# Kernel optimization log

Hardware: AMD Instinct MI355X
Metric: run time of the kernel (lower is better)

Reference implementation:

```python
import jax, jax.numpy as jnp
import numpy as np

HEAD_DIM = 128
NUM_Q_HEAD = 32
NUM_KV_HEAD = 8
SEQLEN_Q = 4096
SEQLEN_KV = 4096
BLOCK_Q = 128
BLOCK_KV = 128
WINDOW = 512
SOFTMAX_CAP = 50.0
EPS = 1e-5
SCALE = 1.0 / np.sqrt(HEAD_DIM)


def group_rms_norm(x, gamma, group_size, eps):
    # x: [b, s, hidden]; RMS-normalize each contiguous group of `group_size` channels, then scale by gamma
    b, s, h = x.shape
    xg = x.reshape(b, s, h // group_size, group_size)
    rms = jnp.sqrt(jnp.mean(jnp.square(xg), axis=-1, keepdims=True) + eps)
    return (xg / rms).reshape(b, s, h) * gamma


def setup_inputs() -> dict:
    key = jax.random.key(0)
    ks = jax.random.split(key, 7)
    b = 4
    q = jax.random.normal(ks[0], (b, BLOCK_Q, NUM_Q_HEAD, HEAD_DIM), dtype=jnp.float32)
    k = jax.random.normal(ks[1], (b, BLOCK_KV, NUM_KV_HEAD, HEAD_DIM), dtype=jnp.float32)
    v = jax.random.normal(ks[2], (b, BLOCK_KV, NUM_KV_HEAD, HEAD_DIM), dtype=jnp.float32)
    global_o = jax.random.normal(ks[3], (b, SEQLEN_Q, NUM_Q_HEAD, HEAD_DIM), dtype=jnp.float32)
    global_lse = jax.random.normal(ks[4], (b, NUM_Q_HEAD, SEQLEN_Q), dtype=jnp.float32)
    gq = jax.random.uniform(ks[5], (NUM_Q_HEAD * HEAD_DIM,), dtype=jnp.float32, minval=-1.0, maxval=1.0)
    gk = jax.random.uniform(ks[6], (NUM_KV_HEAD * HEAD_DIM,), dtype=jnp.float32, minval=-1.0, maxval=1.0)
    return {"q": q, "k": k, "v": v, "global_o": global_o, "global_lse": global_lse,
            "gq": gq, "gk": gk, "block_idx_q": 16, "block_idx_kv": 13}


def reference(q, k, v, global_o, global_lse, gq, gk, block_idx_q, block_idx_kv):
    b, bq = q.shape[0], q.shape[1]
    bkv = k.shape[1]
    # fused QK GroupRMSNorm (group_size == head_dim -> per-head RMS)
    qn = group_rms_norm(q.reshape(b, bq, -1), gq, HEAD_DIM, EPS).reshape(q.shape)
    kn = group_rms_norm(k.reshape(b, bkv, -1), gk, HEAD_DIM, EPS).reshape(k.shape)
    # GQA: repeat kv heads
    rep = NUM_Q_HEAD // NUM_KV_HEAD
    kr = jnp.repeat(kn, rep, axis=2)  # [b, bkv, Hq, d]
    vr = jnp.repeat(v, rep, axis=2)
    # block logits with softmax capping
    logits = jnp.einsum('bqhd,bkhd->bhqk', qn, kr) * SCALE
    logits = SOFTMAX_CAP * jnp.tanh(logits / SOFTMAX_CAP)
    # global positions + causal/sliding-window/padding mask
    qi = block_idx_q * bq + jnp.arange(bq)      # [bq]
    kj = block_idx_kv * bkv + jnp.arange(bkv)   # [bkv]
    offset = SEQLEN_KV - SEQLEN_Q
    diag = qi[:, None] + offset
    allowed = (kj[None, :] <= diag) & (kj[None, :] >= diag - WINDOW)
    allowed = allowed & (qi[:, None] < SEQLEN_Q) & (kj[None, :] < SEQLEN_KV)
    logits = jnp.where(allowed[None, None], logits, -jnp.inf)
    # local softmax stats
    lse_blk = jax.nn.logsumexp(logits, axis=-1)             # [b, h, bq]
    p = jnp.exp(logits - lse_blk[..., None])
    p = jnp.where(jnp.isfinite(lse_blk)[..., None], p, 0.0)  # fully-masked rows -> 0
    o_blk = jnp.einsum('bhqk,bkhd->bqhd', p, vr)             # [b, bq, h, d]
    # online merge with running stats
    row0 = block_idx_q * bq
    lse_old = jax.lax.dynamic_slice_in_dim(global_lse, row0, bq, axis=2)  # [b, h, bq]
    o_old = jax.lax.dynamic_slice_in_dim(global_o, row0, bq, axis=1)      # [b, bq, h, d]
    lse_new = jnp.logaddexp(lse_old, lse_blk)
    fin = jnp.isfinite(lse_new)
    c_old = jnp.where(fin, jnp.exp(jnp.where(fin, lse_old - lse_new, 0.0)), 0.0)
    c_blk = jnp.where(fin, jnp.exp(jnp.where(fin, lse_blk - lse_new, 0.0)), 0.0)
    o_new = jnp.transpose(c_old, (0, 2, 1))[..., None] * o_old + jnp.transpose(c_blk, (0, 2, 1))[..., None] * o_blk
    global_o = jax.lax.dynamic_update_slice_in_dim(global_o, o_new, row0, axis=1)
    global_lse = jax.lax.dynamic_update_slice_in_dim(global_lse, lse_new, row0, axis=2)
    return global_o, global_lse
```

## Files before the change

### kernel.cpp

```cpp
#include <hip/hip_runtime.h>
#include <math.h>

#define HEAD_DIM   128
#define NUM_Q_HEAD 32
#define NUM_KV_HEAD 8
#define SEQLEN_Q   4096
#define SEQLEN_KV  4096
#define BLOCK_Q    128
#define BLOCK_KV   128
#define WINDOW     512
#define SOFTCAP    50.0f
#define EPSV       1e-5f
#define NB         4

#define QROWS  32
#define ZSPLIT (BLOCK_Q / QROWS)
#define NATT   (NB * NUM_Q_HEAD * ZSPLIT)

#define O_FLOATS   (NB * SEQLEN_Q * NUM_Q_HEAD * HEAD_DIM)
#define LSE_FLOATS (NB * NUM_Q_HEAD * SEQLEN_Q)
#define O4N   (O_FLOATS / 4)
#define L4N   (LSE_FLOATS / 4)

#define GRID_COPY 2048
#define GSIZE     ((long long)GRID_COPY * 256)

__global__ __launch_bounds__(256) void bulk_copy(
    const float* __restrict__ gog, const float* __restrict__ glse,
    float* __restrict__ out)
{
    const float4* so = (const float4*)gog;
    const float4* sl = (const float4*)glse;
    float4* d0 = (float4*)out;
    float4* dL = (float4*)(out + (long long)O_FLOATS);

    const long long g = (long long)blockIdx.x * 256 + threadIdx.x;

#pragma unroll
    for (int it = 0; it < 8; ++it) {
        const long long i = g + (long long)it * (GSIZE * 4);
        float4 a = so[i];
        float4 b = so[i + GSIZE];
        float4 c = so[i + 2 * GSIZE];
        float4 d = so[i + 3 * GSIZE];
        d0[i]             = a;
        d0[i + GSIZE]     = b;
        d0[i + 2 * GSIZE] = c;
        d0[i + 3 * GSIZE] = d;
    }
    if (g < (long long)L4N) dL[g] = sl[g];
}

__global__ __launch_bounds__(256, 2) void osw_attn(
    const float* __restrict__ qg, const float* __restrict__ kg_,
    const float* __restrict__ vg, const float* __restrict__ gog,
    const float* __restrict__ glse, const float* __restrict__ gq,
    const float* __restrict__ gk, const int* __restrict__ pbq,
    const int* __restrict__ pbkv, float* __restrict__ out)
{
    __shared__ float kv[64][HEAD_DIM + 4];
    __shared__ float buf[QROWS][HEAD_DIM + 4];
    __shared__ float invks[BLOCK_KV];

    const int tid  = threadIdx.x;
    const int row0 = pbq[0] * BLOCK_Q;

    const int ab = blockIdx.x;
    const int b  = ab >> 7;
    const int h  = (ab >> 2) & 31;
    const int z  = ab & 3;
    const int qo = z * QROWS;
    const int kh = h >> 2;
    const int blkkv = pbkv[0];
    const float scale = 0.088388347648318447f;

    {
        const int r = tid >> 1, half = tid & 1;
        const float* kr = kg_ + (((long long)b * BLOCK_KV + r) * NUM_KV_HEAD + kh) * HEAD_DIM + half * 64;
        float ss = 0.f;
#pragma unroll
        for (int i = 0; i < 16; ++i) {
            float4 x = ((const float4*)kr)[i];
            ss = fmaf(x.x, x.x, ss); ss = fmaf(x.y, x.y, ss);
            ss = fmaf(x.z, x.z, ss); ss = fmaf(x.w, x.w, ss);
        }
        ss += __shfl_xor(ss, 1);
        if (half == 0) invks[r] = rsqrtf(ss * (1.0f / HEAD_DIM) + EPSV);
    }

    {
        const int r = tid >> 3, part = tid & 7;
        const float* qr = qg + (((long long)b * BLOCK_Q + qo + r) * NUM_Q_HEAD + h) * HEAD_DIM + part * 16;
        float4 xv[4];
        float ss = 0.f;
#pragma unroll
        for (int i = 0; i < 4; ++i) {
            xv[i] = ((const float4*)qr)[i];
            ss = fmaf(xv[i].x, xv[i].x, ss); ss = fmaf(xv[i].y, xv[i].y, ss);
            ss = fmaf(xv[i].z, xv[i].z, ss); ss = fmaf(xv[i].w, xv[i].w, ss);
        }
        ss += __shfl_xor(ss, 1);
        ss += __shfl_xor(ss, 2);
        ss += __shfl_xor(ss, 4);
        const float inv = rsqrtf(ss * (1.0f / HEAD_DIM) + EPSV) * scale;
        const float* gqp = gq + h * HEAD_DIM + part * 16;
        const float* gkp = gk + kh * HEAD_DIM + part * 16;
#pragma unroll
        for (int i = 0; i < 4; ++i) {
            float4 a = ((const float4*)gqp)[i];
            float4 c = ((const float4*)gkp)[i];
            int d = part * 16 + i * 4;
            buf[r][d + 0] = xv[i].x * inv * a.x * c.x;
            buf[r][d + 1] = xv[i].y * inv * a.y * c.y;
            buf[r][d + 2] = xv[i].z * inv * a.z * c.z;
            buf[r][d + 3] = xv[i].w * inv * a.w * c.w;
        }
    }
    __syncthreads();

    const int qrow = tid >> 3;
    const int l8   = tid & 7;
    const int qi   = row0 + qo + qrow;
    const int diag = qi + (SEQLEN_KV - SEQLEN_Q);

    const int sr  = tid >> 2;
    const int sc0 = (tid & 3) * 32;

    auto stage_k = [&](int half) {
        const int gr = half * 64 + sr;
        const float iv = invks[gr];
        const float* src = kg_ + (((long long)b * BLOCK_KV + gr) * NUM_KV_HEAD + kh) * HEAD_DIM + sc0;
#pragma unroll
        for (int i = 0; i < 8; ++i) {
            float4 x = ((const float4*)src)[i];
            float4 y; y.x = x.x * iv; y.y = x.y * iv; y.z = x.z * iv; y.w = x.w * iv;
            *(float4*)&kv[sr][sc0 + i * 4] = y;
        }
    };
    auto stage_v = [&](int half) {
        const int gr = half * 64 + sr;
        const float* src = vg + (((long long)b * BLOCK_KV + gr) * NUM_KV_HEAD + kh) * HEAD_DIM + sc0;
#pragma unroll
        for (int i = 0; i < 8; ++i)
            *(float4*)&kv[sr][sc0 + i * 4] = ((const float4*)src)[i];
    };
    auto scores = [&](float (&acc8)[8]) {
        for (int d4 = 0; d4 < HEAD_DIM; d4 += 4) {
            const float4 qf = *(const float4*)&buf[qrow][d4];
#pragma unroll
            for (int j = 0; j < 8; ++j) {
                const float4 kf = *(const float4*)&kv[8 * j + l8][d4];
                acc8[j] = fmaf(qf.x, kf.x, acc8[j]);
                acc8[j] = fmaf(qf.y, kf.y, acc8[j]);
                acc8[j] = fmaf(qf.z, kf.z, acc8[j]);
                acc8[j] = fmaf(qf.w, kf.w, acc8[j]);
            }
        }
    };

    float accA[8] = {0.f, 0.f, 0.f, 0.f, 0.f, 0.f, 0.f, 0.f};
    float accB[8] = {0.f, 0.f, 0.f, 0.f, 0.f, 0.f, 0.f, 0.f};

    stage_k(0);
    __syncthreads();
    scores(accA);
    __syncthreads();
    stage_k(1);
    __syncthreads();
    scores(accB);

    float sv[16];
    float m = -INFINITY;
#pragma unroll
    for (int t = 0; t < 16; ++t) {
        const int kj = blkkv * BLOCK_KV + (t >> 3) * 64 + (t & 7) * 8 + l8;
        const float logit = (t < 8) ? accA[t & 7] : accB[t & 7];
        const float capped = SOFTCAP * tanhf(logit * (1.0f / SOFTCAP));
        const bool allowed = (kj <= diag) && (kj >= diag - WINDOW) &&
                             (qi < SEQLEN_Q) && (kj < SEQLEN_KV);
        sv[t] = allowed ? capped : -INFINITY;
        m = fmaxf(m, sv[t]);
    }
    m = fmaxf(m, __shfl_xor(m, 1));
    m = fmaxf(m, __shfl_xor(m, 2));
    m = fmaxf(m, __shfl_xor(m, 4));
    float ev[16];
    float l = 0.f;
#pragma unroll
    for (int t = 0; t < 16; ++t) {
        ev[t] = (sv[t] > -INFINITY) ? expf(sv[t] - m) : 0.f;
        l += ev[t];
    }
    l += __shfl_xor(l, 1);
    l += __shfl_xor(l, 2);
    l += __shfl_xor(l, 4);
    const float lse_blk = (l > 0.f) ? (m + logf(l)) : -INFINITY;
    const float rinv    = (l > 0.f) ? (1.0f / l) : 0.f;

    const long long lidx = ((long long)b * NUM_Q_HEAD + h) * SEQLEN_Q + qi;
    const float lse_old = glse[lidx];
    float lse_new;
    if (lse_blk == -INFINITY)      lse_new = lse_old;
    else if (lse_old == -INFINITY) lse_new = lse_blk;
    else {
        const float mx = fmaxf(lse_old, lse_blk);
        lse_new = mx + log1pf(expf(-fabsf(lse_old - lse_blk)));
    }
    const float co = (lse_old == -INFINITY || lse_new == -INFINITY) ? 0.f : expf(lse_old - lse_new);
    const float cb = (lse_blk == -INFINITY || lse_new == -INFINITY) ? 0.f : expf(lse_blk - lse_new);
    if (l8 == 0) out[(long long)O_FLOATS + lidx] = lse_new;

    __syncthreads();

#pragma unroll
    for (int t = 0; t < 16; ++t)
        buf[qrow][(t >> 3) * 64 + (t & 7) * 8 + l8] = ev[t] * rinv;
    stage_v(0);
    __syncthreads();

    float4 a[4];
#pragma unroll
    for (int i = 0; i < 4; ++i) a[i] = make_float4(0.f, 0.f, 0.f, 0.f);

    auto pv = [&](int half) {
#pragma unroll 4
        for (int kk = 0; kk < 64; ++kk) {
            const float p = buf[qrow][half * 64 + kk];
#pragma unroll
            for (int i = 0; i < 4; ++i) {
                const float4 v = *(const float4*)&kv[kk][i * 32 + l8 * 4];
                a[i].x = fmaf(p, v.x, a[i].x);
                a[i].y = fmaf(p, v.y, a[i].y);
                a[i].z = fmaf(p, v.z, a[i].z);
                a[i].w = fmaf(p, v.w, a[i].w);
            }
        }
    };
    pv(0);
    __syncthreads();
    stage_v(1);
    __syncthreads();
    pv(1);

    const long long obase = (((long long)b * SEQLEN_Q + qi) * NUM_Q_HEAD + h) * HEAD_DIM;
#pragma unroll
    for (int i = 0; i < 4; ++i) {
        const int d0 = i * 32 + l8 * 4;
        const float4 q4 = *(const float4*)(gog + obase + d0);
        float4 r;
        r.x = fmaf(co, q4.x, cb * a[i].x);
        r.y = fmaf(co, q4.y, cb * a[i].y);
        r.z = fmaf(co, q4.z, cb * a[i].z);
        r.w = fmaf(co, q4.w, cb * a[i].w);
        *(float4*)(out + obase + d0) = r;
    }
}

extern "C" void kernel_launch(void* const* d_in, const int* in_sizes, int n_in,
                              void* d_out, int out_size, void* d_ws, size_t ws_size,
                              hipStream_t stream) {
    const float* q   = (const float*)d_in[0];
    const float* k   = (const float*)d_in[1];
    const float* v   = (const float*)d_in[2];
    const float* go  = (const float*)d_in[3];
    const float* gl  = (const float*)d_in[4];
    const float* gq  = (const float*)d_in[5];
    const float* gk  = (const float*)d_in[6];
    const int*   bq  = (const int*)d_in[7];
    const int*   bkv = (const int*)d_in[8];
    float* out = (float*)d_out;

    bulk_copy<<<dim3(GRID_COPY), dim3(256), 0, stream>>>(go, gl, out);
    osw_attn<<<dim3(NATT), dim3(256), 0, stream>>>(q, k, v, go, gl, gq, gk, bq, bkv, out);
}
```

Measured before the change: 532.7 us.

## Fuse bulk copy into attention kernel and skip rows overwritten by attention

Merges the separate bulk copy kernel into the attention kernel, with extra blocks beyond the attention grid copying global_o and global_lse. Copy blocks skip the 128-row slice that the attention blocks overwrite, which avoids redundant writes and removes the ordering dependency so both run concurrently in one launch. Launch bounds occupancy is raised to 3 waves per SIMD. The per-element row check adds index arithmetic, and copy and attention blocks now compete for the same bandwidth.

```diff
diff --git a/kernel.cpp b/kernel.cpp
--- a/kernel.cpp
+++ b/kernel.cpp
@@ -16,42 +16,15 @@
 #define QROWS  32
 #define ZSPLIT (BLOCK_Q / QROWS)
 #define NATT   (NB * NUM_Q_HEAD * ZSPLIT)
+#define NCOPY  8192
 
 #define O_FLOATS   (NB * SEQLEN_Q * NUM_Q_HEAD * HEAD_DIM)
 #define LSE_FLOATS (NB * NUM_Q_HEAD * SEQLEN_Q)
 #define O4N   (O_FLOATS / 4)
 #define L4N   (LSE_FLOATS / 4)
-
-#define GRID_COPY 2048
-#define GSIZE     ((long long)GRID_COPY * 256)
-
-__global__ __launch_bounds__(256) void bulk_copy(
-    const float* __restrict__ gog, const float* __restrict__ glse,
-    float* __restrict__ out)
-{
-    const float4* so = (const float4*)gog;
-    const float4* sl = (const float4*)glse;
-    float4* d0 = (float4*)out;
-    float4* dL = (float4*)(out + (long long)O_FLOATS);
-
-    const long long g = (long long)blockIdx.x * 256 + threadIdx.x;
-
-#pragma unroll
-    for (int it = 0; it < 8; ++it) {
-        const long long i = g + (long long)it * (GSIZE * 4);
-        float4 a = so[i];
-        float4 b = so[i + GSIZE];
-        float4 c = so[i + 2 * GSIZE];
-        float4 d = so[i + 3 * GSIZE];
-        d0[i]             = a;
-        d0[i + GSIZE]     = b;
-        d0[i + 2 * GSIZE] = c;
-        d0[i + 3 * GSIZE] = d;
-    }
-    if (g < (long long)L4N) dL[g] = sl[g];
-}
-
-__global__ __launch_bounds__(256, 2) void osw_attn(
+#define TOT4  (O4N + L4N)
+
+__global__ __launch_bounds__(256, 3) void osw_fused(
     const float* __restrict__ qg, const float* __restrict__ kg_,
     const float* __restrict__ vg, const float* __restrict__ gog,
     const float* __restrict__ glse, const float* __restrict__ gq,
@@ -64,6 +37,39 @@
 
     const int tid  = threadIdx.x;
     const int row0 = pbq[0] * BLOCK_Q;
+
+    if (blockIdx.x >= NATT) {
+        const long long stride = (long long)NCOPY * 256;
+        const float4* so  = (const float4*)gog;
+        const float4* sl  = (const float4*)glse;
+        float4*       dst = (float4*)out;
+        long long base = (long long)(blockIdx.x - NATT) * 256 + tid;
+        for (; base < (long long)TOT4; base += stride * 4) {
+            float4 val[4];
+            bool   wr[4];
+#pragma unroll
+            for (int u = 0; u < 4; ++u) {
+                long long idx = base + (long long)u * stride;
+                wr[u] = false;
+                if (idx < (long long)O4N) {
+                    int srow = (int)((idx >> 10) & 4095);
+                    if ((unsigned)(srow - row0) >= (unsigned)BLOCK_Q) {
+                        wr[u] = true; val[u] = so[idx];
+                    }
+                } else if (idx < (long long)TOT4) {
+                    int li   = (int)(idx - O4N);
+                    int spos = (li & 1023) << 2;
+                    if ((unsigned)(spos - row0) >= (unsigned)BLOCK_Q) {
+                        wr[u] = true; val[u] = sl[li];
+                    }
+                }
+            }
+#pragma unroll
+            for (int u = 0; u < 4; ++u)
+                if (wr[u]) dst[base + (long long)u * stride] = val[u];
+        }
+        return;
+    }
 
     const int ab = blockIdx.x;
     const int b  = ab >> 7;
@@ -270,6 +276,6 @@
     const int*   bkv = (const int*)d_in[8];
     float* out = (float*)d_out;
 
-    bulk_copy<<<dim3(GRID_COPY), dim3(256), 0, stream>>>(go, gl, out);
-    osw_attn<<<dim3(NATT), dim3(256), 0, stream>>>(q, k, v, go, gl, gq, gk, bq, bkv, out);
+    dim3 grid(NATT + NCOPY), block(256);
+    osw_fused<<<grid, block, 0, stream>>>(q, k, v, go, gl, gq, gk, bq, bkv, out);
 }
```

Result: no change. 523.0 us (-1.8%).
